# Performance work log

Hardware: AMD Instinct MI355X
Metric: run time of the kernel (lower is better)

Reference implementation:

```python
import jax, jax.numpy as jnp
import numpy as np

B, T, D = 4, 4096, 64

def setup_inputs() -> dict:
    key = jax.random.key(0)
    k1, k2, k3 = jax.random.split(key, 3)
    x = jax.random.normal(k1, (B, T, D), dtype=jnp.float32)
    # att_dense1 kernel (zeros init in source; use small random for a meaningful baseline)
    W1 = jax.random.normal(k2, (D, D), dtype=jnp.float32) * 0.05
    b1 = jnp.zeros((D,), dtype=jnp.float32)
    # att_dense2 kernel: glorot_normal
    W2 = jax.random.normal(k3, (D, D), dtype=jnp.float32) * jnp.sqrt(2.0 / (D + D))
    b2 = jnp.zeros((D,), dtype=jnp.float32)
    return {"x": x, "W1": W1, "b1": b1, "W2": W2, "b2": b2}

def reference(x, W1, b1, W2, b2):
    # Per-timestep MLP: Dense(D, softmax) -> Dense(D, tanh)
    h1 = jax.nn.softmax(jnp.einsum('btd,de->bte', x, W1) + b1, axis=-1)
    encoded = jnp.tanh(jnp.einsum('btd,de->bte', h1, W2) + b2)  # [B,T,D]
    # scores[b,i,j] = <x[b,i], encoded[b,j]>
    scores = jnp.einsum('bid,bjd->bij', x, encoded)             # [B,T,T]
    attention = jax.nn.softmax(scores, axis=-1)
    # K.permute_dimensions(attention,(0,2,1)) then batch_dot with x:
    # out[b,i,d] = sum_j attention[b,j,i] * x[b,j,d]
    return jnp.einsum('bji,bjd->bid', attention, x)             # [B,T,D]
```

## Files before the change

kernel.cpp:

```cpp
#include <hip/hip_runtime.h>


typedef _Float16 f16;
typedef __attribute__((ext_vector_type(8))) _Float16 f16x8;
typedef __attribute__((ext_vector_type(4))) _Float16 f16x4;
typedef __attribute__((ext_vector_type(4))) float f32x4;

#define TT 4096
#define BB 4
#define BT (BB*TT)
#define SPLIT_A 16

#define MFMA32(A,B,C) __builtin_amdgcn_mfma_f32_16x16x32_f16(A,B,C,0,0,0)
#define MFMA16(A,B,C) __builtin_amdgcn_mfma_f32_16x16x16f16(A,B,C,0,0,0)

#if __has_builtin(__builtin_amdgcn_exp2f)
#define EXP2F(x) __builtin_amdgcn_exp2f(x)
#else
#define EXP2F(x) exp2f(x)
#endif

#define LOG2E 1.4426950408889634f

__global__ __launch_bounds__(256) void k_wpack(
    const float* __restrict__ W1, const float* __restrict__ W2,
    f16* __restrict__ w1fh, f16* __restrict__ w1fl,
    f16* __restrict__ w2fh, f16* __restrict__ w2fl) {
  int tid = threadIdx.x;
#pragma unroll
  for (int k2 = 0; k2 < 2; ++k2) {
    int idx = tid * 2 + k2;
    int l15 = idx & 15, quad = (idx >> 4) & 3, kc = (idx >> 6) & 1, mtW = idx >> 7;
    f16 h8[8], l8[8];
#pragma unroll
    for (int t = 0; t < 8; ++t) {
      float v = W1[(size_t)(kc * 32 + quad * 8 + t) * 64 + mtW * 16 + l15];
      f16 h = (f16)v;
      h8[t] = h; l8[t] = (f16)(v - (float)h);
    }
    *(f16x8*)(w1fh + (size_t)idx * 8) = *(f16x8*)h8;
    *(f16x8*)(w1fl + (size_t)idx * 8) = *(f16x8*)l8;
  }
#pragma unroll
  for (int k4 = 0; k4 < 4; ++k4) {
    int idx = tid * 4 + k4;
    int l15 = idx & 15, quad = (idx >> 4) & 3, kt = (idx >> 6) & 3, mt2 = idx >> 8;
    f16 h4[4], l4[4];
#pragma unroll
    for (int t = 0; t < 4; ++t) {
      float v = W2[(size_t)(kt * 16 + quad * 4 + t) * 64 + mt2 * 16 + l15];
      f16 h = (f16)v;
      h4[t] = h; l4[t] = (f16)(v - (float)h);
    }
    *(f16x4*)(w2fh + (size_t)idx * 4) = *(f16x4*)h4;
    *(f16x4*)(w2fl + (size_t)idx * 4) = *(f16x4*)l4;
  }
}

__global__ __launch_bounds__(256, 1) void k_encode(
    const float* __restrict__ x,
    const float* __restrict__ b1, const float* __restrict__ b2,
    const f16* __restrict__ w1fh, const f16* __restrict__ w1fl,
    const f16* __restrict__ w2fh, const f16* __restrict__ w2fl,
    f16* __restrict__ ench, f16* __restrict__ encl,
    f16* __restrict__ xafh, f16* __restrict__ xafl, f16* __restrict__ xtf,
    float* __restrict__ Zbuf) {
  __shared__ float xS[4][16][68];
  __shared__ float encS[4][16][68];
  int tid = threadIdx.x;
  int w = tid >> 6, lane = tid & 63, quad = lane >> 4, l15 = lane & 15;
  if (tid < 64) Zbuf[blockIdx.x * 64 + tid] = 0.f;
  int slice = blockIdx.x * 4 + w;
  int base = slice * 16;
  f16x8 w1h[4][2], w1l[4][2];
#pragma unroll
  for (int mt = 0; mt < 4; ++mt)
#pragma unroll
    for (int kc = 0; kc < 2; ++kc) {
      size_t off = (size_t)(((mt * 2 + kc) * 4 + quad) * 16 + l15) * 8;
      w1h[mt][kc] = *(const f16x8*)(w1fh + off);
      w1l[mt][kc] = *(const f16x8*)(w1fl + off);
    }
  f16x4 w2h[4][4], w2l[4][4];
#pragma unroll
  for (int mt = 0; mt < 4; ++mt)
#pragma unroll
    for (int kt = 0; kt < 4; ++kt) {
      size_t off = (size_t)(((mt * 4 + kt) * 4 + quad) * 16 + l15) * 4;
      w2h[mt][kt] = *(const f16x4*)(w2fh + off);
      w2l[mt][kt] = *(const f16x4*)(w2fl + off);
    }
  f16x8 xbh[2], xbl[2];
#pragma unroll
  for (int kc = 0; kc < 2; ++kc) {
    const float4* p = (const float4*)(x + (size_t)(base + l15) * 64 + kc * 32 + quad * 8);
    float4 v0 = p[0], v1 = p[1];
    float v[8] = {v0.x, v0.y, v0.z, v0.w, v1.x, v1.y, v1.z, v1.w};
    f16 h8[8], l8[8];
#pragma unroll
    for (int t = 0; t < 8; ++t) {
      f16 h = (f16)v[t];
      h8[t] = h; l8[t] = (f16)(v[t] - (float)h);
    }
    xbh[kc] = *(f16x8*)h8;
    xbl[kc] = *(f16x8*)l8;
    size_t off = (size_t)slice * 1024 + kc * 512 + quad * 128 + l15 * 8;
    *(f16x8*)(xafh + off) = xbh[kc];
    *(f16x8*)(xafl + off) = xbl[kc];
    *(float4*)&xS[w][l15][kc * 32 + quad * 8] = v0;
    *(float4*)&xS[w][l15][kc * 32 + quad * 8 + 4] = v1;
  }
  f32x4 acc1[4];
#pragma unroll
  for (int mt = 0; mt < 4; ++mt) {
    f32x4 z = {0.f, 0.f, 0.f, 0.f};
    acc1[mt] = z;
  }
#pragma unroll
  for (int kc = 0; kc < 2; ++kc)
#pragma unroll
    for (int mt = 0; mt < 4; ++mt) {
      acc1[mt] = MFMA32(w1h[mt][kc], xbh[kc], acc1[mt]);
      acc1[mt] = MFMA32(w1h[mt][kc], xbl[kc], acc1[mt]);
      acc1[mt] = MFMA32(w1l[mt][kc], xbh[kc], acc1[mt]);
    }
  float h1[4][4];
#pragma unroll
  for (int mt = 0; mt < 4; ++mt) {
    float4 bv = *(const float4*)(b1 + mt * 16 + quad * 4);
    h1[mt][0] = acc1[mt][0] + bv.x;
    h1[mt][1] = acc1[mt][1] + bv.y;
    h1[mt][2] = acc1[mt][2] + bv.z;
    h1[mt][3] = acc1[mt][3] + bv.w;
  }
  float m1 = h1[0][0];
#pragma unroll
  for (int mt = 0; mt < 4; ++mt)
#pragma unroll
    for (int r = 0; r < 4; ++r) m1 = fmaxf(m1, h1[mt][r]);
  m1 = fmaxf(m1, __shfl_xor(m1, 16));
  m1 = fmaxf(m1, __shfl_xor(m1, 32));
  float ssum = 0.f;
  float ev[4][4];
#pragma unroll
  for (int mt = 0; mt < 4; ++mt)
#pragma unroll
    for (int r = 0; r < 4; ++r) {
      ev[mt][r] = EXP2F((h1[mt][r] - m1) * LOG2E);
      ssum += ev[mt][r];
    }
  ssum += __shfl_xor(ssum, 16);
  ssum += __shfl_xor(ssum, 32);
  float rs = __builtin_amdgcn_rcpf(ssum);
  f16x4 p1h[4], p1l[4];
#pragma unroll
  for (int mt = 0; mt < 4; ++mt)
#pragma unroll
    for (int r = 0; r < 4; ++r) {
      float p = ev[mt][r] * rs;
      f16 h = (f16)p;
      p1h[mt][r] = h;
      p1l[mt][r] = (f16)(p - (float)h);
    }
  f32x4 acc2[4];
#pragma unroll
  for (int mt = 0; mt < 4; ++mt) {
    f32x4 z = {0.f, 0.f, 0.f, 0.f};
    acc2[mt] = z;
  }
#pragma unroll
  for (int kt = 0; kt < 4; ++kt)
#pragma unroll
    for (int mt = 0; mt < 4; ++mt) {
      acc2[mt] = MFMA16(w2h[mt][kt], p1h[kt], acc2[mt]);
      acc2[mt] = MFMA16(w2h[mt][kt], p1l[kt], acc2[mt]);
      acc2[mt] = MFMA16(w2l[mt][kt], p1h[kt], acc2[mt]);
    }
#pragma unroll
  for (int mt = 0; mt < 4; ++mt) {
    float4 bv = *(const float4*)(b2 + mt * 16 + quad * 4);
    float bb[4] = {bv.x, bv.y, bv.z, bv.w};
    float o4[4];
#pragma unroll
    for (int r = 0; r < 4; ++r) {
      float hv = acc2[mt][r] + bb[r];
      float ex = EXP2F(hv * (2.0f * LOG2E));
      float th = 1.0f - 2.0f * __builtin_amdgcn_rcpf(ex + 1.0f);
      o4[r] = th * LOG2E;
    }
    *(float4*)&encS[w][l15][mt * 16 + quad * 4] = *(float4*)o4;
  }
#pragma unroll
  for (int k = 0; k < 2; ++k) {
    int e = k * 64 + lane;
    int n = e & 15, quad2 = (e >> 4) & 3, kc = e >> 6;
    const float4* p = (const float4*)&encS[w][n][kc * 32 + quad2 * 8];
    float4 v0 = p[0], v1 = p[1];
    float v[8] = {v0.x, v0.y, v0.z, v0.w, v1.x, v1.y, v1.z, v1.w};
    f16 h8[8], l8[8];
#pragma unroll
    for (int t = 0; t < 8; ++t) {
      f16 h = (f16)v[t];
      h8[t] = h; l8[t] = (f16)(v[t] - (float)h);
    }
    *(f16x8*)(ench + ((size_t)slice * 128 + e) * 8) = *(f16x8*)h8;
    *(f16x8*)(encl + ((size_t)slice * 128 + e) * 8) = *(f16x8*)l8;
  }
  int b = slice >> 8, ls = slice & 255;
#pragma unroll
  for (int k = 0; k < 4; ++k) {
    f16 p8[8];
#pragma unroll
    for (int t = 0; t < 4; ++t) {
      float v = xS[w][k * 4 + t][lane];
      f16 h = (f16)v;
      p8[t] = h; p8[4 + t] = (f16)(v - (float)h);
    }
    size_t off = ((((size_t)b * (TT / 16) + ls) * 4 + k) * 64 + lane) * 8;
    *(f16x8*)(xtf + off) = *(f16x8*)p8;
  }
}

__global__ __launch_bounds__(512, 4) void k_statsM(
    const f16* __restrict__ xafh, const f16* __restrict__ ench,
    float* __restrict__ Zbuf) {
  int tid = threadIdx.x;
  int w = tid >> 6, lane = tid & 63, quad = lane >> 4, l15 = lane & 15;
  int jb = blockIdx.x * 256 + w * 32;
  int b = jb >> 12;
  f16x8 xa[2][2];
#pragma unroll
  for (int mt = 0; mt < 2; ++mt)
#pragma unroll
    for (int kc = 0; kc < 2; ++kc) {
      size_t off = (size_t)((jb >> 4) + mt) * 1024 + kc * 512 + quad * 128 + l15 * 8;
      xa[mt][kc] = *(const f16x8*)(xafh + off);
    }
  float l_run[8];
#pragma unroll
  for (int s = 0; s < 8; ++s) l_run[s] = 0.f;
  int i0 = blockIdx.y * (TT / SPLIT_A);
  size_t ebase = (size_t)((b * TT + i0) >> 4) * 1024 + quad * 128 + l15 * 8;
  const f16* pEh = ench + ebase;
  for (int it = 0; it < TT / SPLIT_A / 64; ++it) {
    f32x4 acc[2][4];
#pragma unroll
    for (int mt = 0; mt < 2; ++mt)
#pragma unroll
      for (int nt = 0; nt < 4; ++nt) {
        f32x4 z = {0.f, 0.f, 0.f, 0.f};
        acc[mt][nt] = z;
      }
#pragma unroll
    for (int kc = 0; kc < 2; ++kc) {
      f16x8 ebf[4];
#pragma unroll
      for (int nt = 0; nt < 4; ++nt)
        ebf[nt] = *(const f16x8*)(pEh + nt * 1024 + kc * 512);
#pragma unroll
      for (int mt = 0; mt < 2; ++mt)
#pragma unroll
        for (int nt = 0; nt < 4; ++nt)
          acc[mt][nt] = MFMA32(xa[mt][kc], ebf[nt], acc[mt][nt]);
    }
#pragma unroll
    for (int mt = 0; mt < 2; ++mt)
#pragma unroll
      for (int r = 0; r < 4; ++r)
        l_run[mt * 4 + r] += EXP2F(acc[mt][0][r]) + EXP2F(acc[mt][1][r]) +
                             EXP2F(acc[mt][2][r]) + EXP2F(acc[mt][3][r]);
    pEh += 4096;
  }
#pragma unroll
  for (int s = 0; s < 8; ++s) {
    float l = l_run[s];
#pragma unroll
    for (int off = 1; off < 16; off <<= 1) l += __shfl_xor(l, off);
    l_run[s] = l;
  }
  if (l15 == 0) {
#pragma unroll
    for (int mt = 0; mt < 2; ++mt)
#pragma unroll
      for (int r = 0; r < 4; ++r)
        atomicAdd(Zbuf + jb + mt * 16 + quad * 4 + r, l_run[mt * 4 + r]);
  }
}

__global__ __launch_bounds__(512, 4) void k_outB(
    const f16* __restrict__ xafh, const f16* __restrict__ xafl,
    const f16* __restrict__ xtf,
    const f16* __restrict__ ench, const f16* __restrict__ encl,
    const float* __restrict__ Zv, float* __restrict__ slabs, int jlen) {
  int tid = threadIdx.x;
  int w = tid >> 6, lane = tid & 63, quad = lane >> 4, l15 = lane & 15;
  int ibase = blockIdx.x * 256;
  int iw = ibase + w * 32;
  int b = ibase >> 12;
  f16x8 ebr[2][2][2];
#pragma unroll
  for (int nt = 0; nt < 2; ++nt)
#pragma unroll
    for (int kc = 0; kc < 2; ++kc) {
      size_t off = (size_t)((iw >> 4) + nt) * 1024 + kc * 512 + quad * 128 + l15 * 8;
      ebr[nt][kc][0] = *(const f16x8*)(ench + off);
      ebr[nt][kc][1] = *(const f16x8*)(encl + off);
    }
  f32x4 oacc[2][4];
#pragma unroll
  for (int nt = 0; nt < 2; ++nt)
#pragma unroll
    for (int mtb = 0; mtb < 4; ++mtb) {
      f32x4 z = {0.f, 0.f, 0.f, 0.f};
      oacc[nt][mtb] = z;
    }
  int jt0 = blockIdx.y * jlen;
  int nit = jlen / 16;
  size_t jf0 = (size_t)b * TT + jt0;
  const f16* pAh = xafh + (jf0 >> 4) * 1024 + quad * 128 + l15 * 8;
  const f16* pAl = xafl + (jf0 >> 4) * 1024 + quad * 128 + l15 * 8;
  const f16* pPV = xtf + ((size_t)b * (TT / 16) + (jt0 >> 4)) * 2048 +
                   quad * 512 + l15 * 8;
  const float* pZ = Zv + jf0 + quad * 4;
  f16x8 cah[2], cal[2];
  cah[0] = *(const f16x8*)(pAh);       cah[1] = *(const f16x8*)(pAh + 512);
  cal[0] = *(const f16x8*)(pAl);       cal[1] = *(const f16x8*)(pAl + 512);
  pAh += 1024; pAl += 1024;
  for (int t = 0; t < nit; ++t) {
    f16x8 pv[4];
#pragma unroll
    for (int mtb = 0; mtb < 4; ++mtb)
      pv[mtb] = *(const f16x8*)(pPV + mtb * 128);
    float rz[4];
#pragma unroll
    for (int r = 0; r < 4; ++r)
      rz[r] = __builtin_amdgcn_rcpf(pZ[r]);
    f16x8 nah[2], nal[2];
    nah[0] = *(const f16x8*)(pAh);     nah[1] = *(const f16x8*)(pAh + 512);
    nal[0] = *(const f16x8*)(pAl);     nal[1] = *(const f16x8*)(pAl + 512);
    f32x4 sacc[2];
#pragma unroll
    for (int nt = 0; nt < 2; ++nt) {
      f32x4 z = {0.f, 0.f, 0.f, 0.f};
      sacc[nt] = z;
    }
#pragma unroll
    for (int kc = 0; kc < 2; ++kc)
#pragma unroll
      for (int nt = 0; nt < 2; ++nt) {
        sacc[nt] = MFMA32(cah[kc], ebr[nt][kc][0], sacc[nt]);
        sacc[nt] = MFMA32(cah[kc], ebr[nt][kc][1], sacc[nt]);
        sacc[nt] = MFMA32(cal[kc], ebr[nt][kc][0], sacc[nt]);
      }
    f16x4 pbh[2];
#pragma unroll
    for (int nt = 0; nt < 2; ++nt)
#pragma unroll
      for (int r = 0; r < 4; ++r)
        pbh[nt][r] = (f16)(EXP2F(sacc[nt][r]) * rz[r]);
#pragma unroll
    for (int mtb = 0; mtb < 4; ++mtb) {
      f16x4 bh = {pv[mtb][0], pv[mtb][1], pv[mtb][2], pv[mtb][3]};
      f16x4 bl = {pv[mtb][4], pv[mtb][5], pv[mtb][6], pv[mtb][7]};
#pragma unroll
      for (int nt = 0; nt < 2; ++nt) {
        oacc[nt][mtb] = MFMA16(pbh[nt], bh, oacc[nt][mtb]);
        oacc[nt][mtb] = MFMA16(pbh[nt], bl, oacc[nt][mtb]);
      }
    }
    cah[0] = nah[0]; cah[1] = nah[1];
    cal[0] = nal[0]; cal[1] = nal[1];
    pAh += 1024; pAl += 1024; pPV += 2048; pZ += 16;
  }
  float* slab = slabs + (size_t)blockIdx.y * BT * 64;
#pragma unroll
  for (int nt = 0; nt < 2; ++nt)
#pragma unroll
    for (int r = 0; r < 4; ++r) {
      int i = iw + nt * 16 + quad * 4 + r;
#pragma unroll
      for (int mtb = 0; mtb < 4; ++mtb)
        slab[(size_t)i * 64 + mtb * 16 + l15] = oacc[nt][mtb][r];
    }
}

__global__ __launch_bounds__(256) void k_reduce(const float* __restrict__ slabs,
                                                float* __restrict__ out,
                                                int nsplit) {
  int e = (blockIdx.x * 256 + threadIdx.x) * 4;
  float4 acc = *(const float4*)(slabs + e);
  for (int s = 1; s < nsplit; ++s) {
    float4 v = *(const float4*)(slabs + (size_t)s * BT * 64 + e);
    acc.x += v.x; acc.y += v.y; acc.z += v.z; acc.w += v.w;
  }
  *(float4*)(out + e) = acc;
}

extern "C" void kernel_launch(void* const* d_in, const int* in_sizes, int n_in,
                              void* d_out, int out_size, void* d_ws,
                              size_t ws_size, hipStream_t stream) {
  const float* x = (const float*)d_in[0];
  const float* W1 = (const float*)d_in[1];
  const float* b1 = (const float*)d_in[2];
  const float* W2 = (const float*)d_in[3];
  const float* b2 = (const float*)d_in[4];
  float* out = (float*)d_out;

  f16* xafh = (f16*)d_ws;
  f16* xafl = xafh + (size_t)BT * 64;
  f16* xtf  = xafl + (size_t)BT * 64;
  f16* ench = xtf + (size_t)BT * 128;
  f16* encl = ench + (size_t)BT * 64;
  float* Zv = (float*)(encl + (size_t)BT * 64);
  f16* w1fh = (f16*)(Zv + BT);
  f16* w1fl = w1fh + 4096;
  f16* w2fh = w1fl + 4096;
  f16* w2fl = w2fh + 4096;
  float* slabs = (float*)(w2fl + 4096);

  size_t base_bytes = (size_t)((char*)slabs - (char*)d_ws);
  size_t slab_bytes = (size_t)BT * 64 * sizeof(float);
  int nsplit = 8;
  while (nsplit > 1 && base_bytes + (size_t)nsplit * slab_bytes > ws_size)
    nsplit >>= 1;

  k_wpack<<<dim3(1), dim3(256), 0, stream>>>(W1, W2, w1fh, w1fl, w2fh, w2fl);
  k_encode<<<dim3(BT / 64), dim3(256), 0, stream>>>(
      x, b1, b2, w1fh, w1fl, w2fh, w2fl, ench, encl, xafh, xafl, xtf, Zv);
  k_statsM<<<dim3(BT / 256, SPLIT_A), dim3(512), 0, stream>>>(xafh, ench, Zv);
  k_outB<<<dim3(BT / 256, nsplit), dim3(512), 0, stream>>>(
      xafh, xafl, xtf, ench, encl, Zv, slabs, TT / nsplit);
  k_reduce<<<dim3(BT * 64 / 1024), dim3(256), 0, stream>>>(slabs, out, nsplit);
}
```

Measured before the change: 141.9 us.

## Fold weight packing into encode, drop PV low half, prefetch PV and Z

Removes the separate weight-packing kernel: k_encode now splits W1 and W2 into fp16 hi/lo parts itself, which saves one launch. In the output kernel, the P·V product now uses only the high fp16 half of x, halving those MFMAs at the cost of some accuracy. The next tile's PV fragments and normalizer Z are now prefetched with a vector load a step ahead, like the A operands, to hide load latency.

```diff
diff --git a/kernel.cpp b/kernel.cpp
--- a/kernel.cpp
+++ b/kernel.cpp
@@ -22,46 +22,10 @@
 
 #define LOG2E 1.4426950408889634f
 
-__global__ __launch_bounds__(256) void k_wpack(
-    const float* __restrict__ W1, const float* __restrict__ W2,
-    f16* __restrict__ w1fh, f16* __restrict__ w1fl,
-    f16* __restrict__ w2fh, f16* __restrict__ w2fl) {
-  int tid = threadIdx.x;
-#pragma unroll
-  for (int k2 = 0; k2 < 2; ++k2) {
-    int idx = tid * 2 + k2;
-    int l15 = idx & 15, quad = (idx >> 4) & 3, kc = (idx >> 6) & 1, mtW = idx >> 7;
-    f16 h8[8], l8[8];
-#pragma unroll
-    for (int t = 0; t < 8; ++t) {
-      float v = W1[(size_t)(kc * 32 + quad * 8 + t) * 64 + mtW * 16 + l15];
-      f16 h = (f16)v;
-      h8[t] = h; l8[t] = (f16)(v - (float)h);
-    }
-    *(f16x8*)(w1fh + (size_t)idx * 8) = *(f16x8*)h8;
-    *(f16x8*)(w1fl + (size_t)idx * 8) = *(f16x8*)l8;
-  }
-#pragma unroll
-  for (int k4 = 0; k4 < 4; ++k4) {
-    int idx = tid * 4 + k4;
-    int l15 = idx & 15, quad = (idx >> 4) & 3, kt = (idx >> 6) & 3, mt2 = idx >> 8;
-    f16 h4[4], l4[4];
-#pragma unroll
-    for (int t = 0; t < 4; ++t) {
-      float v = W2[(size_t)(kt * 16 + quad * 4 + t) * 64 + mt2 * 16 + l15];
-      f16 h = (f16)v;
-      h4[t] = h; l4[t] = (f16)(v - (float)h);
-    }
-    *(f16x4*)(w2fh + (size_t)idx * 4) = *(f16x4*)h4;
-    *(f16x4*)(w2fl + (size_t)idx * 4) = *(f16x4*)l4;
-  }
-}
-
 __global__ __launch_bounds__(256, 1) void k_encode(
     const float* __restrict__ x,
-    const float* __restrict__ b1, const float* __restrict__ b2,
-    const f16* __restrict__ w1fh, const f16* __restrict__ w1fl,
-    const f16* __restrict__ w2fh, const f16* __restrict__ w2fl,
+    const float* __restrict__ W1, const float* __restrict__ b1,
+    const float* __restrict__ W2, const float* __restrict__ b2,
     f16* __restrict__ ench, f16* __restrict__ encl,
     f16* __restrict__ xafh, f16* __restrict__ xafl, f16* __restrict__ xtf,
     float* __restrict__ Zbuf) {
@@ -77,18 +41,30 @@
   for (int mt = 0; mt < 4; ++mt)
 #pragma unroll
     for (int kc = 0; kc < 2; ++kc) {
-      size_t off = (size_t)(((mt * 2 + kc) * 4 + quad) * 16 + l15) * 8;
-      w1h[mt][kc] = *(const f16x8*)(w1fh + off);
-      w1l[mt][kc] = *(const f16x8*)(w1fl + off);
+      f16 h8[8], l8[8];
+#pragma unroll
+      for (int t = 0; t < 8; ++t) {
+        float v = W1[(size_t)(kc * 32 + quad * 8 + t) * 64 + mt * 16 + l15];
+        f16 h = (f16)v;
+        h8[t] = h; l8[t] = (f16)(v - (float)h);
+      }
+      w1h[mt][kc] = *(f16x8*)h8;
+      w1l[mt][kc] = *(f16x8*)l8;
     }
   f16x4 w2h[4][4], w2l[4][4];
 #pragma unroll
   for (int mt = 0; mt < 4; ++mt)
 #pragma unroll
     for (int kt = 0; kt < 4; ++kt) {
-      size_t off = (size_t)(((mt * 4 + kt) * 4 + quad) * 16 + l15) * 4;
-      w2h[mt][kt] = *(const f16x4*)(w2fh + off);
-      w2l[mt][kt] = *(const f16x4*)(w2fl + off);
+      f16 h4[4], l4[4];
+#pragma unroll
+      for (int t = 0; t < 4; ++t) {
+        float v = W2[(size_t)(kt * 16 + quad * 4 + t) * 64 + mt * 16 + l15];
+        f16 h = (f16)v;
+        h4[t] = h; l4[t] = (f16)(v - (float)h);
+      }
+      w2h[mt][kt] = *(f16x4*)h4;
+      w2l[mt][kt] = *(f16x4*)l4;
     }
   f16x8 xbh[2], xbl[2];
 #pragma unroll
@@ -323,21 +299,25 @@
                    quad * 512 + l15 * 8;
   const float* pZ = Zv + jf0 + quad * 4;
   f16x8 cah[2], cal[2];
+  f16x4 cpv[4];
+  float4 cZ;
   cah[0] = *(const f16x8*)(pAh);       cah[1] = *(const f16x8*)(pAh + 512);
   cal[0] = *(const f16x8*)(pAl);       cal[1] = *(const f16x8*)(pAl + 512);
-  pAh += 1024; pAl += 1024;
+#pragma unroll
+  for (int mtb = 0; mtb < 4; ++mtb)
+    cpv[mtb] = *(const f16x4*)(pPV + mtb * 128);
+  cZ = *(const float4*)pZ;
+  pAh += 1024; pAl += 1024; pPV += 2048; pZ += 16;
   for (int t = 0; t < nit; ++t) {
-    f16x8 pv[4];
-#pragma unroll
-    for (int mtb = 0; mtb < 4; ++mtb)
-      pv[mtb] = *(const f16x8*)(pPV + mtb * 128);
-    float rz[4];
-#pragma unroll
-    for (int r = 0; r < 4; ++r)
-      rz[r] = __builtin_amdgcn_rcpf(pZ[r]);
     f16x8 nah[2], nal[2];
+    f16x4 npv[4];
+    float4 nZ;
     nah[0] = *(const f16x8*)(pAh);     nah[1] = *(const f16x8*)(pAh + 512);
     nal[0] = *(const f16x8*)(pAl);     nal[1] = *(const f16x8*)(pAl + 512);
+#pragma unroll
+    for (int mtb = 0; mtb < 4; ++mtb)
+      npv[mtb] = *(const f16x4*)(pPV + mtb * 128);
+    nZ = *(const float4*)pZ;
     f32x4 sacc[2];
 #pragma unroll
     for (int nt = 0; nt < 2; ++nt) {
@@ -352,6 +332,8 @@
         sacc[nt] = MFMA32(cah[kc], ebr[nt][kc][1], sacc[nt]);
         sacc[nt] = MFMA32(cal[kc], ebr[nt][kc][0], sacc[nt]);
       }
+    float rz[4] = {__builtin_amdgcn_rcpf(cZ.x), __builtin_amdgcn_rcpf(cZ.y),
+                   __builtin_amdgcn_rcpf(cZ.z), __builtin_amdgcn_rcpf(cZ.w)};
     f16x4 pbh[2];
 #pragma unroll
     for (int nt = 0; nt < 2; ++nt)
@@ -359,17 +341,15 @@
       for (int r = 0; r < 4; ++r)
         pbh[nt][r] = (f16)(EXP2F(sacc[nt][r]) * rz[r]);
 #pragma unroll
-    for (int mtb = 0; mtb < 4; ++mtb) {
-      f16x4 bh = {pv[mtb][0], pv[mtb][1], pv[mtb][2], pv[mtb][3]};
-      f16x4 bl = {pv[mtb][4], pv[mtb][5], pv[mtb][6], pv[mtb][7]};
-#pragma unroll
-      for (int nt = 0; nt < 2; ++nt) {
-        oacc[nt][mtb] = MFMA16(pbh[nt], bh, oacc[nt][mtb]);
-        oacc[nt][mtb] = MFMA16(pbh[nt], bl, oacc[nt][mtb]);
-      }
-    }
+    for (int mtb = 0; mtb < 4; ++mtb)
+#pragma unroll
+      for (int nt = 0; nt < 2; ++nt)
+        oacc[nt][mtb] = MFMA16(pbh[nt], cpv[mtb], oacc[nt][mtb]);
     cah[0] = nah[0]; cah[1] = nah[1];
     cal[0] = nal[0]; cal[1] = nal[1];
+#pragma unroll
+    for (int mtb = 0; mtb < 4; ++mtb) cpv[mtb] = npv[mtb];
+    cZ = nZ;
     pAh += 1024; pAl += 1024; pPV += 2048; pZ += 16;
   }
   float* slab = slabs + (size_t)blockIdx.y * BT * 64;
@@ -412,11 +392,7 @@
   f16* ench = xtf + (size_t)BT * 128;
   f16* encl = ench + (size_t)BT * 64;
   float* Zv = (float*)(encl + (size_t)BT * 64);
-  f16* w1fh = (f16*)(Zv + BT);
-  f16* w1fl = w1fh + 4096;
-  f16* w2fh = w1fl + 4096;
-  f16* w2fl = w2fh + 4096;
-  float* slabs = (float*)(w2fl + 4096);
+  float* slabs = Zv + BT + 1024;
 
   size_t base_bytes = (size_t)((char*)slabs - (char*)d_ws);
   size_t slab_bytes = (size_t)BT * 64 * sizeof(float);
@@ -424,9 +400,8 @@
   while (nsplit > 1 && base_bytes + (size_t)nsplit * slab_bytes > ws_size)
     nsplit >>= 1;
 
-  k_wpack<<<dim3(1), dim3(256), 0, stream>>>(W1, W2, w1fh, w1fl, w2fh, w2fl);
   k_encode<<<dim3(BT / 64), dim3(256), 0, stream>>>(
-      x, b1, b2, w1fh, w1fl, w2fh, w2fl, ench, encl, xafh, xafl, xtf, Zv);
+      x, W1, b1, W2, b2, ench, encl, xafh, xafl, xtf, Zv);
   k_statsM<<<dim3(BT / 256, SPLIT_A), dim3(512), 0, stream>>>(xafh, ench, Zv);
   k_outB<<<dim3(BT / 256, nsplit), dim3(512), 0, stream>>>(
       xafh, xafl, xtf, ench, encl, Zv, slabs, TT / nsplit);
```

New measurement: 145.4 us. +2.5%, slower.

## Replace split-K slab reduction with atomic output accumulation and drop PV low half

Applied to the files above, without the earlier changes.

The output partials from the split-j kernel are now atomically added straight into the output buffer, which the encode kernel zeroes first, so the separate slab workspace and reduce kernel go away. The PV loop also keeps only the high-f16 half of the packed x values, halving the second-stage MFMAs. It prefetches the next PV and Z values one iteration ahead alongside the A fragments. Dropping the low half lowers precision of the x operand. Float atomics make the summation order nondeterministic.

```diff
diff --git a/kernel.cpp b/kernel.cpp
--- a/kernel.cpp
+++ b/kernel.cpp
@@ -10,6 +10,7 @@
 #define BB 4
 #define BT (BB*TT)
 #define SPLIT_A 16
+#define NSPLIT_B 8
 
 #define MFMA32(A,B,C) __builtin_amdgcn_mfma_f32_16x16x32_f16(A,B,C,0,0,0)
 #define MFMA16(A,B,C) __builtin_amdgcn_mfma_f32_16x16x16f16(A,B,C,0,0,0)
@@ -64,12 +65,18 @@
     const f16* __restrict__ w2fh, const f16* __restrict__ w2fl,
     f16* __restrict__ ench, f16* __restrict__ encl,
     f16* __restrict__ xafh, f16* __restrict__ xafl, f16* __restrict__ xtf,
-    float* __restrict__ Zbuf) {
+    float* __restrict__ Zbuf, float* __restrict__ out) {
   __shared__ float xS[4][16][68];
   __shared__ float encS[4][16][68];
   int tid = threadIdx.x;
   int w = tid >> 6, lane = tid & 63, quad = lane >> 4, l15 = lane & 15;
   if (tid < 64) Zbuf[blockIdx.x * 64 + tid] = 0.f;
+  {
+    float4 z4 = make_float4(0.f, 0.f, 0.f, 0.f);
+#pragma unroll
+    for (int k = 0; k < 4; ++k)
+      ((float4*)out)[(size_t)blockIdx.x * 1024 + k * 256 + tid] = z4;
+  }
   int slice = blockIdx.x * 4 + w;
   int base = slice * 16;
   f16x8 w1h[4][2], w1l[4][2];
@@ -291,7 +298,7 @@
     const f16* __restrict__ xafh, const f16* __restrict__ xafl,
     const f16* __restrict__ xtf,
     const f16* __restrict__ ench, const f16* __restrict__ encl,
-    const float* __restrict__ Zv, float* __restrict__ slabs, int jlen) {
+    const float* __restrict__ Zv, float* __restrict__ out, int jlen) {
   int tid = threadIdx.x;
   int w = tid >> 6, lane = tid & 63, quad = lane >> 4, l15 = lane & 15;
   int ibase = blockIdx.x * 256;
@@ -323,21 +330,25 @@
                    quad * 512 + l15 * 8;
   const float* pZ = Zv + jf0 + quad * 4;
   f16x8 cah[2], cal[2];
+  f16x4 cpv[4];
+  float4 cZ;
   cah[0] = *(const f16x8*)(pAh);       cah[1] = *(const f16x8*)(pAh + 512);
   cal[0] = *(const f16x8*)(pAl);       cal[1] = *(const f16x8*)(pAl + 512);
-  pAh += 1024; pAl += 1024;
+#pragma unroll
+  for (int mtb = 0; mtb < 4; ++mtb)
+    cpv[mtb] = *(const f16x4*)(pPV + mtb * 128);
+  cZ = *(const float4*)pZ;
+  pAh += 1024; pAl += 1024; pPV += 2048; pZ += 16;
   for (int t = 0; t < nit; ++t) {
-    f16x8 pv[4];
-#pragma unroll
-    for (int mtb = 0; mtb < 4; ++mtb)
-      pv[mtb] = *(const f16x8*)(pPV + mtb * 128);
-    float rz[4];
-#pragma unroll
-    for (int r = 0; r < 4; ++r)
-      rz[r] = __builtin_amdgcn_rcpf(pZ[r]);
     f16x8 nah[2], nal[2];
+    f16x4 npv[4];
+    float4 nZ;
     nah[0] = *(const f16x8*)(pAh);     nah[1] = *(const f16x8*)(pAh + 512);
     nal[0] = *(const f16x8*)(pAl);     nal[1] = *(const f16x8*)(pAl + 512);
+#pragma unroll
+    for (int mtb = 0; mtb < 4; ++mtb)
+      npv[mtb] = *(const f16x4*)(pPV + mtb * 128);
+    nZ = *(const float4*)pZ;
     f32x4 sacc[2];
 #pragma unroll
     for (int nt = 0; nt < 2; ++nt) {
@@ -352,6 +363,8 @@
         sacc[nt] = MFMA32(cah[kc], ebr[nt][kc][1], sacc[nt]);
         sacc[nt] = MFMA32(cal[kc], ebr[nt][kc][0], sacc[nt]);
       }
+    float rz[4] = {__builtin_amdgcn_rcpf(cZ.x), __builtin_amdgcn_rcpf(cZ.y),
+                   __builtin_amdgcn_rcpf(cZ.z), __builtin_amdgcn_rcpf(cZ.w)};
     f16x4 pbh[2];
 #pragma unroll
     for (int nt = 0; nt < 2; ++nt)
@@ -359,20 +372,17 @@
       for (int r = 0; r < 4; ++r)
         pbh[nt][r] = (f16)(EXP2F(sacc[nt][r]) * rz[r]);
 #pragma unroll
-    for (int mtb = 0; mtb < 4; ++mtb) {
-      f16x4 bh = {pv[mtb][0], pv[mtb][1], pv[mtb][2], pv[mtb][3]};
-      f16x4 bl = {pv[mtb][4], pv[mtb][5], pv[mtb][6], pv[mtb][7]};
-#pragma unroll
-      for (int nt = 0; nt < 2; ++nt) {
-        oacc[nt][mtb] = MFMA16(pbh[nt], bh, oacc[nt][mtb]);
-        oacc[nt][mtb] = MFMA16(pbh[nt], bl, oacc[nt][mtb]);
-      }
-    }
+    for (int mtb = 0; mtb < 4; ++mtb)
+#pragma unroll
+      for (int nt = 0; nt < 2; ++nt)
+        oacc[nt][mtb] = MFMA16(pbh[nt], cpv[mtb], oacc[nt][mtb]);
     cah[0] = nah[0]; cah[1] = nah[1];
     cal[0] = nal[0]; cal[1] = nal[1];
+#pragma unroll
+    for (int mtb = 0; mtb < 4; ++mtb) cpv[mtb] = npv[mtb];
+    cZ = nZ;
     pAh += 1024; pAl += 1024; pPV += 2048; pZ += 16;
   }
-  float* slab = slabs + (size_t)blockIdx.y * BT * 64;
 #pragma unroll
   for (int nt = 0; nt < 2; ++nt)
 #pragma unroll
@@ -380,20 +390,8 @@
       int i = iw + nt * 16 + quad * 4 + r;
 #pragma unroll
       for (int mtb = 0; mtb < 4; ++mtb)
-        slab[(size_t)i * 64 + mtb * 16 + l15] = oacc[nt][mtb][r];
-    }
-}
-
-__global__ __launch_bounds__(256) void k_reduce(const float* __restrict__ slabs,
-                                                float* __restrict__ out,
-                                                int nsplit) {
-  int e = (blockIdx.x * 256 + threadIdx.x) * 4;
-  float4 acc = *(const float4*)(slabs + e);
-  for (int s = 1; s < nsplit; ++s) {
-    float4 v = *(const float4*)(slabs + (size_t)s * BT * 64 + e);
-    acc.x += v.x; acc.y += v.y; acc.z += v.z; acc.w += v.w;
-  }
-  *(float4*)(out + e) = acc;
+        atomicAdd(out + (size_t)i * 64 + mtb * 16 + l15, oacc[nt][mtb][r]);
+    }
 }
 
 extern "C" void kernel_launch(void* const* d_in, const int* in_sizes, int n_in,
@@ -412,23 +410,15 @@
   f16* ench = xtf + (size_t)BT * 128;
   f16* encl = ench + (size_t)BT * 64;
   float* Zv = (float*)(encl + (size_t)BT * 64);
-  f16* w1fh = (f16*)(Zv + BT);
+  f16* w1fh = (f16*)(Zv + BT + 1024);
   f16* w1fl = w1fh + 4096;
   f16* w2fh = w1fl + 4096;
   f16* w2fl = w2fh + 4096;
-  float* slabs = (float*)(w2fl + 4096);
-
-  size_t base_bytes = (size_t)((char*)slabs - (char*)d_ws);
-  size_t slab_bytes = (size_t)BT * 64 * sizeof(float);
-  int nsplit = 8;
-  while (nsplit > 1 && base_bytes + (size_t)nsplit * slab_bytes > ws_size)
-    nsplit >>= 1;
 
   k_wpack<<<dim3(1), dim3(256), 0, stream>>>(W1, W2, w1fh, w1fl, w2fh, w2fl);
   k_encode<<<dim3(BT / 64), dim3(256), 0, stream>>>(
-      x, b1, b2, w1fh, w1fl, w2fh, w2fl, ench, encl, xafh, xafl, xtf, Zv);
+      x, b1, b2, w1fh, w1fl, w2fh, w2fl, ench, encl, xafh, xafl, xtf, Zv, out);
   k_statsM<<<dim3(BT / 256, SPLIT_A), dim3(512), 0, stream>>>(xafh, ench, Zv);
-  k_outB<<<dim3(BT / 256, nsplit), dim3(512), 0, stream>>>(
-      xafh, xafl, xtf, ench, encl, Zv, slabs, TT / nsplit);
-  k_reduce<<<dim3(BT * 64 / 1024), dim3(256), 0, stream>>>(slabs, out, nsplit);
+  k_outB<<<dim3(BT / 256, NSPLIT_B), dim3(512), 0, stream>>>(
+      xafh, xafl, xtf, ench, encl, Zv, out, TT / NSPLIT_B);
 }
```

After: 152.0 us. 1.07x slower.
